# Optimization experiments

Measured on AMD Instinct MI355X. Metric: run time of the kernel, lower is better.

The kernel has to match this reference:

```python
import jax, jax.numpy as jnp
import numpy as np

B, S, H = 8, 1024, 1024
NH, DH = 16, 64
F_DIM, E, TOPK = 4096, 8, 2
EPS = 1e-5


def setup_inputs() -> dict:
    key = jax.random.key(0)
    ks = jax.random.split(key, 12)
    s = 0.02
    return {
        "x": jax.random.normal(ks[0], (B, S, H), jnp.float32),
        "ln1_w": jnp.ones((H,), jnp.float32),
        "ln1_b": jnp.zeros((H,), jnp.float32),
        "ln2_w": jnp.ones((H,), jnp.float32),
        "ln2_b": jnp.zeros((H,), jnp.float32),
        "in_proj_w": jax.random.normal(ks[1], (3 * H, H), jnp.float32) * s,
        "in_proj_b": jnp.zeros((3 * H,), jnp.float32),
        "out_proj_w": jax.random.normal(ks[2], (H, H), jnp.float32) * s,
        "out_proj_b": jnp.zeros((H,), jnp.float32),
        "gate_w": jax.random.normal(ks[3], (E, H), jnp.float32) * s,
        "gate_b": jnp.zeros((E,), jnp.float32),
        "w1": jax.random.normal(ks[4], (E, H, F_DIM), jnp.float32) * s,
        "b1": jnp.zeros((E, F_DIM), jnp.float32),
        "w2": jax.random.normal(ks[5], (E, F_DIM, H), jnp.float32) * s,
        "b2": jnp.zeros((E, H), jnp.float32),
    }


def _layernorm(x, w, b):
    mu = jnp.mean(x, axis=-1, keepdims=True)
    var = jnp.var(x, axis=-1, keepdims=True)
    return (x - mu) * jax.lax.rsqrt(var + EPS) * w + b


def reference(x, ln1_w, ln1_b, ln2_w, ln2_b, in_proj_w, in_proj_b,
              out_proj_w, out_proj_b, gate_w, gate_b, w1, b1, w2, b2):
    # --- attention sub-block ---
    xn = _layernorm(x, ln1_w, ln1_b)
    qkv = xn @ in_proj_w.T + in_proj_b                     # [B,S,3H]
    q, k, v = jnp.split(qkv, 3, axis=-1)
    q = q.reshape(B, S, NH, DH).transpose(0, 2, 1, 3)      # [B,NH,S,DH]
    k = k.reshape(B, S, NH, DH).transpose(0, 2, 1, 3)
    v = v.reshape(B, S, NH, DH).transpose(0, 2, 1, 3)
    scores = jnp.einsum("bhqd,bhkd->bhqk", q, k) / jnp.sqrt(jnp.float32(DH))
    attn = jax.nn.softmax(scores, axis=-1)
    ctx = jnp.einsum("bhqk,bhkd->bhqd", attn, v)
    ctx = ctx.transpose(0, 2, 1, 3).reshape(B, S, H)
    x = x + ctx @ out_proj_w.T + out_proj_b

    # --- MoE sub-block (dense compute-all-experts, top-k combine) ---
    xn2 = _layernorm(x, ln2_w, ln2_b)
    logits = xn2 @ gate_w.T + gate_b                       # [B,S,E]
    topk_vals, topk_idx = jax.lax.top_k(logits, TOPK)      # [B,S,K]
    probs = jax.nn.softmax(topk_vals, axis=-1)
    hid = jax.nn.gelu(jnp.einsum("bsh,ehf->bsef", xn2, w1) + b1, approximate=False)
    expert_out = jnp.einsum("bsef,efh->bseh", hid, w2) + b2  # [B,S,E,H]
    selected = jnp.take_along_axis(expert_out, topk_idx[..., None], axis=2)  # [B,S,K,H]
    moe_out = jnp.sum(probs[..., None] * selected, axis=2)
    return x + moe_out
```

## Files before the change

kernel.cpp:

```cpp
#include <hip/hip_runtime.h>
#include <math.h>

typedef unsigned short u16;
typedef short short8 __attribute__((ext_vector_type(8)));
typedef float f32x4 __attribute__((ext_vector_type(4)));
typedef unsigned short us4 __attribute__((ext_vector_type(4)));

#define NTOK 8192
#define NEXP 8

__device__ __forceinline__ u16 f2bf(float f) {
  union { float f; unsigned u; } v; v.f = f;
  unsigned r = v.u + 0x7FFFu + ((v.u >> 16) & 1u);
  return (u16)(r >> 16);
}
__device__ __forceinline__ float bf2f(u16 u) {
  union { unsigned u; float f; } v; v.u = ((unsigned)u) << 16; return v.f;
}
__device__ __forceinline__ void gload16(const u16* src, u16* ldsDst) {
  __builtin_amdgcn_global_load_lds(
    (const __attribute__((address_space(1))) unsigned int*)(const void*)src,
    (__attribute__((address_space(3))) unsigned int*)(void*)ldsDst, 16, 0, 0);
}
__device__ __forceinline__ float gelu_f(float v) {
  float ax = fabsf(v) * 0.70710678f;
  float t = __builtin_amdgcn_rcpf(1.0f + 0.3275911f * ax);
  float p = t * (0.254829592f + t * (-0.284496736f + t * (1.421413741f +
            t * (-1.453152027f + t * 1.061405429f))));
  float er = 1.0f - p * __expf(-ax * ax);
  er = copysignf(er, v);
  return 0.5f * v * (1.0f + er);
}

__global__ void cast_kernel(const float* __restrict__ in, u16* __restrict__ out, int n4) {
  int i = blockIdx.x * blockDim.x + threadIdx.x;
  if (i < n4) {
    float4 v = ((const float4*)in)[i];
    us4 o;
    o[0] = f2bf(v.x); o[1] = f2bf(v.y); o[2] = f2bf(v.z); o[3] = f2bf(v.w);
    ((us4*)out)[i] = o;
  }
}

__global__ void transpose_cast(const float* __restrict__ in, u16* __restrict__ out, int R, int C) {
  __shared__ float tile[64][65];
  const size_t eoff = (size_t)blockIdx.z * (size_t)R * (size_t)C;
  in += eoff; out += eoff;
  const int rb = blockIdx.y * 64, cb = blockIdx.x * 64;
  const int tid = threadIdx.x;
  const int lr4 = tid >> 4;
  const int lc4 = (tid & 15) * 4;
#pragma unroll
  for (int p = 0; p < 4; ++p) {
    float4 v = *(const float4*)&in[(size_t)(rb + p * 16 + lr4) * C + cb + lc4];
    tile[p * 16 + lr4][lc4 + 0] = v.x;
    tile[p * 16 + lr4][lc4 + 1] = v.y;
    tile[p * 16 + lr4][lc4 + 2] = v.z;
    tile[p * 16 + lr4][lc4 + 3] = v.w;
  }
  __syncthreads();
  const int oc = tid >> 3;
  const int orr = (tid & 7) * 8;
#pragma unroll
  for (int p = 0; p < 2; ++p) {
    int c = p * 32 + oc;
    short8 o;
#pragma unroll
    for (int j = 0; j < 8; ++j) o[j] = (short)f2bf(tile[orr + j][c]);
    *(short8*)&out[(size_t)(cb + c) * R + rb + orr] = o;
  }
}

__global__ void ln1_kernel(const float* __restrict__ x, const float* __restrict__ w,
                           const float* __restrict__ b, u16* __restrict__ xn) {
  const int t = blockIdx.x, tid = threadIdx.x;
  __shared__ float red[8];
  float4 v = ((const float4*)(x + (size_t)t * 1024))[tid];
  float s  = v.x + v.y + v.z + v.w;
  float sq = v.x*v.x + v.y*v.y + v.z*v.z + v.w*v.w;
#pragma unroll
  for (int m = 1; m < 64; m <<= 1) { s += __shfl_xor(s, m, 64); sq += __shfl_xor(sq, m, 64); }
  if ((tid & 63) == 0) { red[tid >> 6] = s; red[4 + (tid >> 6)] = sq; }
  __syncthreads();
  float S = red[0] + red[1] + red[2] + red[3];
  float Q = red[4] + red[5] + red[6] + red[7];
  float mu  = S * (1.0f / 1024.0f);
  float var = Q * (1.0f / 1024.0f) - mu * mu;
  float inv = rsqrtf(var + 1e-5f);
  float4 wv = ((const float4*)w)[tid];
  float4 bv = ((const float4*)b)[tid];
  us4 o;
  o[0] = f2bf((v.x - mu) * inv * wv.x + bv.x);
  o[1] = f2bf((v.y - mu) * inv * wv.y + bv.y);
  o[2] = f2bf((v.z - mu) * inv * wv.z + bv.z);
  o[3] = f2bf((v.w - mu) * inv * wv.w + bv.w);
  ((us4*)(xn + (size_t)t * 1024))[tid] = o;
}

__global__ void ln2_gate_kernel(const float* __restrict__ x2, const float* __restrict__ w,
                                const float* __restrict__ b, const float* __restrict__ gw,
                                const float* __restrict__ gb, u16* __restrict__ xn2,
                                int* __restrict__ cnt, int* __restrict__ list_tok,
                                float* __restrict__ list_prob, int* __restrict__ tok2slot) {
  const int t = blockIdx.x, tid = threadIdx.x;
  __shared__ float red[8];
  __shared__ float logits[NEXP];
  __shared__ float xrow[1024];
  float4 v = ((const float4*)(x2 + (size_t)t * 1024))[tid];
  float s  = v.x + v.y + v.z + v.w;
  float sq = v.x*v.x + v.y*v.y + v.z*v.z + v.w*v.w;
#pragma unroll
  for (int m = 1; m < 64; m <<= 1) { s += __shfl_xor(s, m, 64); sq += __shfl_xor(sq, m, 64); }
  if ((tid & 63) == 0) { red[tid >> 6] = s; red[4 + (tid >> 6)] = sq; }
  __syncthreads();
  float S = red[0] + red[1] + red[2] + red[3];
  float Q = red[4] + red[5] + red[6] + red[7];
  float mu  = S * (1.0f / 1024.0f);
  float var = Q * (1.0f / 1024.0f) - mu * mu;
  float inv = rsqrtf(var + 1e-5f);
  float4 wv = ((const float4*)w)[tid];
  float4 bv = ((const float4*)b)[tid];
  float n0 = (v.x - mu) * inv * wv.x + bv.x;
  float n1 = (v.y - mu) * inv * wv.y + bv.y;
  float n2 = (v.z - mu) * inv * wv.z + bv.z;
  float n3 = (v.w - mu) * inv * wv.w + bv.w;
  xrow[tid*4+0] = n0; xrow[tid*4+1] = n1; xrow[tid*4+2] = n2; xrow[tid*4+3] = n3;
  us4 o; o[0] = f2bf(n0); o[1] = f2bf(n1); o[2] = f2bf(n2); o[3] = f2bf(n3);
  ((us4*)(xn2 + (size_t)t * 1024))[tid] = o;
  __syncthreads();
  int e = tid >> 5, l32 = tid & 31;
  const float* gwe = gw + e * 1024;
  float part = 0.0f;
  for (int i = l32; i < 1024; i += 32) part += xrow[i] * gwe[i];
#pragma unroll
  for (int m = 1; m < 32; m <<= 1) part += __shfl_xor(part, m, 64);
  if (l32 == 0) logits[e] = part + gb[e];
  __syncthreads();
  if (tid == 0) {
    float v0 = -1e30f; int e0 = 0;
#pragma unroll
    for (int i = 0; i < NEXP; ++i) { float L = logits[i]; if (L > v0) { v0 = L; e0 = i; } }
    float v1 = -1e30f; int e1 = 0;
#pragma unroll
    for (int i = 0; i < NEXP; ++i) { if (i == e0) continue; float L = logits[i]; if (L > v1) { v1 = L; e1 = i; } }
    float texp = expf(v1 - v0);
    float p0 = 1.0f / (1.0f + texp);
    float p1 = texp / (1.0f + texp);
    int s0 = atomicAdd(&cnt[e0], 1);
    list_tok[e0 * NTOK + s0] = t; list_prob[e0 * NTOK + s0] = p0;
    int s1 = atomicAdd(&cnt[e1], 1);
    list_tok[e1 * NTOK + s1] = t; list_prob[e1 * NTOK + s1] = p1;
    if (tok2slot) {
      tok2slot[2 * t]     = e0 * NTOK + s0;
      tok2slot[2 * t + 1] = e1 * NTOK + s1;
    }
  }
}

__global__ void plan_kernel(const int* __restrict__ cnt, int* __restrict__ meta) {
  if (threadIdx.x == 0) {
    int base = 0, p = 0;
    for (int e = 0; e < NEXP; ++e) {
      meta[e] = base;
      int c = cnt[e];
      base += c;
      int nm = (c + 127) >> 7;
      for (int i = 0; i < nm; ++i) { meta[16 + 2 * p] = e; meta[17 + 2 * p] = i << 7; ++p; }
    }
    meta[8] = p;
  }
}

__launch_bounds__(256)
__global__ void attn_kernel(const u16* __restrict__ qkv, u16* __restrict__ ctx) {
  const int bh = blockIdx.y;
  const int b = bh >> 4, h = bh & 15;
  const int q0 = blockIdx.x * 64;
  const int tokBase = b * 1024;
  __shared__ __align__(16) u16 Qs[64 * 72];
  __shared__ __align__(16) u16 Ks[64 * 72];
  __shared__ __align__(16) u16 Vts[64 * 72];
  __shared__ __align__(16) u16 Ps[64 * 72];
  const int tid = threadIdx.x;
  const int wave = tid >> 6, lane = tid & 63, g = lane >> 4, lr = lane & 15;

  {
    int r = tid >> 2, d0 = (tid & 3) * 16;
    const u16* src = qkv + (size_t)(tokBase + q0 + r) * 3072 + h * 64 + d0;
    *(short8*)&Qs[r * 72 + d0]     = *(const short8*)src;
    *(short8*)&Qs[r * 72 + d0 + 8] = *(const short8*)(src + 8);
  }
  __syncthreads();
  short8 aq0 = *(const short8*)&Qs[(wave * 16 + lr) * 72 + g * 8];
  short8 aq1 = *(const short8*)&Qs[(wave * 16 + lr) * 72 + 32 + g * 8];

  const f32x4 zf = {0.f, 0.f, 0.f, 0.f};
  f32x4 Ofr[4] = {zf, zf, zf, zf};
  float m_run[4], l_run[4];
#pragma unroll
  for (int r = 0; r < 4; ++r) { m_run[r] = -1e30f; l_run[r] = 0.f; }

  for (int kt = 0; kt < 1024; kt += 64) {
    __syncthreads();
    {
      int r = tid >> 2, d0 = (tid & 3) * 16;
      const u16* ksrc = qkv + (size_t)(tokBase + kt + r) * 3072 + 1024 + h * 64 + d0;
      *(short8*)&Ks[r * 72 + d0]     = *(const short8*)ksrc;
      *(short8*)&Ks[r * 72 + d0 + 8] = *(const short8*)(ksrc + 8);
      const u16* vsrc = qkv + (size_t)(tokBase + kt + r) * 3072 + 2048 + h * 64 + d0;
      short8 v0 = *(const short8*)vsrc, v1 = *(const short8*)(vsrc + 8);
#pragma unroll
      for (int j = 0; j < 8; ++j) Vts[(d0 + j) * 72 + r] = (u16)v0[j];
#pragma unroll
      for (int j = 0; j < 8; ++j) Vts[(d0 + 8 + j) * 72 + r] = (u16)v1[j];
    }
    __syncthreads();
    f32x4 sf[4];
#pragma unroll
    for (int n = 0; n < 4; ++n) sf[n] = zf;
#pragma unroll
    for (int n = 0; n < 4; ++n) {
      short8 bk0 = *(const short8*)&Ks[(n * 16 + lr) * 72 + g * 8];
      short8 bk1 = *(const short8*)&Ks[(n * 16 + lr) * 72 + 32 + g * 8];
      sf[n] = __builtin_amdgcn_mfma_f32_16x16x32_bf16(aq0, bk0, sf[n], 0, 0, 0);
      sf[n] = __builtin_amdgcn_mfma_f32_16x16x32_bf16(aq1, bk1, sf[n], 0, 0, 0);
    }
#pragma unroll
    for (int n = 0; n < 4; ++n)
#pragma unroll
      for (int r = 0; r < 4; ++r) sf[n][r] *= 0.125f;
    float mnew[4], sc[4];
#pragma unroll
    for (int r = 0; r < 4; ++r) {
      float t0 = fmaxf(fmaxf(sf[0][r], sf[1][r]), fmaxf(sf[2][r], sf[3][r]));
#pragma unroll
      for (int msk = 1; msk < 16; msk <<= 1) t0 = fmaxf(t0, __shfl_xor(t0, msk, 64));
      mnew[r] = fmaxf(m_run[r], t0);
      sc[r] = __expf(m_run[r] - mnew[r]);
      m_run[r] = mnew[r];
    }
#pragma unroll
    for (int n = 0; n < 4; ++n)
#pragma unroll
      for (int r = 0; r < 4; ++r) sf[n][r] = __expf(sf[n][r] - mnew[r]);
#pragma unroll
    for (int r = 0; r < 4; ++r) {
      float s0 = sf[0][r] + sf[1][r] + sf[2][r] + sf[3][r];
#pragma unroll
      for (int msk = 1; msk < 16; msk <<= 1) s0 += __shfl_xor(s0, msk, 64);
      l_run[r] = l_run[r] * sc[r] + s0;
    }
#pragma unroll
    for (int nd = 0; nd < 4; ++nd)
#pragma unroll
      for (int r = 0; r < 4; ++r) Ofr[nd][r] *= sc[r];
#pragma unroll
    for (int n = 0; n < 4; ++n)
#pragma unroll
      for (int r = 0; r < 4; ++r)
        Ps[(wave * 16 + g * 4 + r) * 72 + n * 16 + lr] = f2bf(sf[n][r]);
    __syncthreads();
    short8 ap0 = *(const short8*)&Ps[(wave * 16 + lr) * 72 + g * 8];
    short8 ap1 = *(const short8*)&Ps[(wave * 16 + lr) * 72 + 32 + g * 8];
#pragma unroll
    for (int nd = 0; nd < 4; ++nd) {
      short8 bv0 = *(const short8*)&Vts[(nd * 16 + lr) * 72 + g * 8];
      short8 bv1 = *(const short8*)&Vts[(nd * 16 + lr) * 72 + 32 + g * 8];
      Ofr[nd] = __builtin_amdgcn_mfma_f32_16x16x32_bf16(ap0, bv0, Ofr[nd], 0, 0, 0);
      Ofr[nd] = __builtin_amdgcn_mfma_f32_16x16x32_bf16(ap1, bv1, Ofr[nd], 0, 0, 0);
    }
  }
#pragma unroll
  for (int nd = 0; nd < 4; ++nd)
#pragma unroll
    for (int r = 0; r < 4; ++r) {
      int tok = tokBase + q0 + wave * 16 + g * 4 + r;
      int col = h * 64 + nd * 16 + lr;
      ctx[(size_t)tok * 1024 + col] = f2bf(Ofr[nd][r] / l_run[r]);
    }
}

template<int EPI>
__launch_bounds__(256)
__global__ void gemm128(const u16* __restrict__ Abase, const u16* __restrict__ Bbase,
                        int K, int lda, int N, int ldc,
                        const float* __restrict__ bias,
                        const float* __restrict__ resid,
                        float* __restrict__ outF,
                        u16* __restrict__ outB,
                        const int* __restrict__ cnt,
                        const int* __restrict__ meta,
                        const int* __restrict__ list_tok,
                        const float* __restrict__ list_prob) {
  const int gx = gridDim.x, gy = gridDim.y;
  int nwg = gx * gy;
  int orig = blockIdx.x + blockIdx.y * gx;
  int q8 = nwg >> 3, r8 = nwg & 7, xcd = orig & 7, lid = orig >> 3;
  int wg = (xcd < r8 ? xcd * (q8 + 1) : r8 * (q8 + 1) + (xcd - r8) * q8) + lid;
  const int bx = wg % gx, by = wg / gx;
  const int n0 = bx * 128;

  int m0, e = 0, M = NTOK, slotBase = 0;
  const u16* Bw = Bbase;
  const float* biasp = bias;
  if constexpr (EPI >= 2) {
    if (by >= meta[8]) return;
    e = meta[16 + 2 * by];
    m0 = meta[17 + 2 * by];
    M = cnt[e];
    slotBase = meta[e];
    Bw += (size_t)e * (size_t)N * (size_t)K;
    biasp = bias + (size_t)e * N;
  } else {
    m0 = by * 128;
  }

  __shared__ __align__(16) u16 As[2][8192];
  __shared__ __align__(16) u16 Bs[2][8192];

  const int tid = threadIdx.x;
  const int wave = tid >> 6, lane = tid & 63, g = lane >> 4, lr = lane & 15;
  const int wm = wave >> 1, wn = wave & 1;

  unsigned aoff[4], boff[4];
#pragma unroll
  for (int i = 0; i < 4; ++i) {
    int ci = i * 256 + tid;
    int row = ci >> 3, c = ci & 7;
    int lc = c ^ (row & 7);
    int arow;
    if constexpr (EPI == 2) {
      int ridx = m0 + row; if (ridx > M - 1) ridx = M - 1;
      arow = list_tok[e * NTOK + ridx];
    } else if constexpr (EPI >= 3) {
      int ridx = m0 + row; if (ridx > M - 1) ridx = M - 1;
      arow = slotBase + ridx;
    } else {
      arow = m0 + row;
    }
    aoff[i] = (unsigned)arow * (unsigned)lda + (unsigned)(lc << 3);
    boff[i] = (unsigned)(n0 + row) * (unsigned)K + (unsigned)(lc << 3);
  }

  const int NT = K >> 6;

#define STAGE(T) do { int _t = (T); if (_t < NT) { int _b = _t & 1; int _kt = _t << 6; \
    _Pragma("unroll") for (int i = 0; i < 4; ++i) { \
      gload16(Abase + aoff[i] + _kt, &As[_b][(i * 256 + wave * 64) << 3]); \
      gload16(Bw + boff[i] + _kt, &Bs[_b][(i * 256 + wave * 64) << 3]); } } } while (0)

  const int sw = lr & 7;
  const int arb = (wm * 64 + lr) * 64;
  const int brb = (wn * 64 + lr) * 64;
  const int sk0 = (g ^ sw) * 8;
  const int sk1 = ((4 + g) ^ sw) * 8;

  const f32x4 zf = {0.f, 0.f, 0.f, 0.f};
  f32x4 acc[4][4];
#pragma unroll
  for (int m = 0; m < 4; ++m)
#pragma unroll
    for (int n = 0; n < 4; ++n) acc[m][n] = zf;

  STAGE(0);
  asm volatile("s_waitcnt vmcnt(0)" ::: "memory");
  __builtin_amdgcn_s_barrier();

  for (int t = 0; t < NT; ++t) {
    STAGE(t + 1);
    const u16* Ab = As[t & 1];
    const u16* Bb = Bs[t & 1];
    short8 af[4][2], bf[4][2];
#pragma unroll
    for (int m = 0; m < 4; ++m) {
      af[m][0] = *(const short8*)&Ab[arb + m * 1024 + sk0];
      af[m][1] = *(const short8*)&Ab[arb + m * 1024 + sk1];
    }
#pragma unroll
    for (int n = 0; n < 4; ++n) {
      bf[n][0] = *(const short8*)&Bb[brb + n * 1024 + sk0];
      bf[n][1] = *(const short8*)&Bb[brb + n * 1024 + sk1];
    }
    __builtin_amdgcn_s_setprio(1);
#pragma unroll
    for (int kk = 0; kk < 2; ++kk)
#pragma unroll
      for (int m = 0; m < 4; ++m)
#pragma unroll
        for (int n = 0; n < 4; ++n)
          acc[m][n] = __builtin_amdgcn_mfma_f32_16x16x32_bf16(af[m][kk], bf[n][kk], acc[m][n], 0, 0, 0);
    __builtin_amdgcn_s_setprio(0);
    asm volatile("s_waitcnt vmcnt(0)" ::: "memory");
    __builtin_amdgcn_s_barrier();
  }
#undef STAGE

#pragma unroll
  for (int m = 0; m < 4; ++m) {
    int rloc = wm * 64 + m * 16 + g * 4;
#pragma unroll
    for (int n = 0; n < 4; ++n) {
      int gc = n0 + wn * 64 + n * 16 + lr;
      float bcol = biasp[gc];
#pragma unroll
      for (int r = 0; r < 4; ++r) {
        int ridx = m0 + rloc + r;
        float vv = acc[m][n][r] + bcol;
        if constexpr (EPI == 0) {
          outB[(size_t)ridx * ldc + gc] = f2bf(vv);
        } else if constexpr (EPI == 1) {
          size_t off = (size_t)ridx * ldc + gc;
          outF[off] = vv + resid[off];
        } else if constexpr (EPI == 2) {
          if (ridx < M)
            outB[(size_t)(slotBase + ridx) * ldc + gc] = f2bf(gelu_f(vv));
        } else if constexpr (EPI == 3) {
          if (ridx < M)
            outB[(size_t)(slotBase + ridx) * ldc + gc] = f2bf(vv);
        } else {
          if (ridx < M) {
            int tok = list_tok[e * NTOK + ridx];
            float p = list_prob[e * NTOK + ridx];
            atomicAdd(&outF[(size_t)tok * ldc + gc], vv * p);
          }
        }
      }
    }
  }
}

__global__ void combine_kernel(const u16* __restrict__ part, const int* __restrict__ cnt,
                               const int* __restrict__ tok2slot, const float* __restrict__ lprb,
                               float* __restrict__ out) {
  const int t = blockIdx.x, tid = threadIdx.x;
  __shared__ int base[NEXP];
  if (tid == 0) {
    int b = 0;
#pragma unroll
    for (int j = 0; j < NEXP; ++j) { base[j] = b; b += cnt[j]; }
  }
  __syncthreads();
  int c0 = tok2slot[2 * t], c1 = tok2slot[2 * t + 1];
  float p0 = lprb[c0], p1 = lprb[c1];
  int g0 = base[c0 >> 13] + (c0 & 8191);
  int g1 = base[c1 >> 13] + (c1 & 8191);
  us4 a = ((const us4*)(part + (size_t)g0 * 1024))[tid];
  us4 b = ((const us4*)(part + (size_t)g1 * 1024))[tid];
  float4 o = ((const float4*)(out + (size_t)t * 1024))[tid];
  o.x += p0 * bf2f(a[0]) + p1 * bf2f(b[0]);
  o.y += p0 * bf2f(a[1]) + p1 * bf2f(b[1]);
  o.z += p0 * bf2f(a[2]) + p1 * bf2f(b[2]);
  o.w += p0 * bf2f(a[3]) + p1 * bf2f(b[3]);
  ((float4*)(out + (size_t)t * 1024))[tid] = o;
}

extern "C" void kernel_launch(void* const* d_in, const int* in_sizes, int n_in,
                              void* d_out, int out_size, void* d_ws, size_t ws_size,
                              hipStream_t stream) {
  const float* x    = (const float*)d_in[0];
  const float* ln1w = (const float*)d_in[1];
  const float* ln1b = (const float*)d_in[2];
  const float* ln2w = (const float*)d_in[3];
  const float* ln2b = (const float*)d_in[4];
  const float* inw  = (const float*)d_in[5];
  const float* inb  = (const float*)d_in[6];
  const float* outw = (const float*)d_in[7];
  const float* outb = (const float*)d_in[8];
  const float* gw   = (const float*)d_in[9];
  const float* gb   = (const float*)d_in[10];
  const float* w1   = (const float*)d_in[11];
  const float* b1   = (const float*)d_in[12];
  const float* w2   = (const float*)d_in[13];
  const float* b2   = (const float*)d_in[14];
  float* out = (float*)d_out;
  char* ws = (char*)d_ws;

  u16* xn1 = (u16*)(ws + 0);
  u16* qkv = (u16*)(ws + 16777216);
  u16* ctx = (u16*)(ws + 67108864);
  u16* hid = (u16*)(ws + 0);
  u16* xn2 = (u16*)(ws + 134217728);
  u16* w1t = (u16*)(ws + 150994944);
  u16* winb  = (u16*)(ws + 218103808);
  u16* woutb = (u16*)(ws + 224395264);
  u16* w2t = (u16*)(ws + 134217728);
  u16* part = (u16*)(ws + 201326592);

  const bool bigWS = ws_size >= 235475456ull;
  int *cnt, *meta, *ltok, *t2s; float* lprb;
  if (bigWS) {
    cnt  = (int*)(ws + 234881024);
    meta = (int*)(ws + 234883072);
    ltok = (int*)(ws + 234887168);
    lprb = (float*)(ws + 235149312);
    t2s  = (int*)(ws + 235411456);
  } else {
    cnt  = (int*)(ws + 226492416);
    meta = (int*)(ws + 226494464);
    ltok = (int*)(ws + 226498560);
    lprb = (float*)(ws + 226760704);
    t2s  = nullptr;
  }

  cast_kernel<<<3072, 256, 0, stream>>>(inw, winb, 786432);
  cast_kernel<<<1024, 256, 0, stream>>>(outw, woutb, 262144);
  transpose_cast<<<dim3(64, 16, 8), 256, 0, stream>>>(w1, w1t, 1024, 4096);

  ln1_kernel<<<8192, 256, 0, stream>>>(x, ln1w, ln1b, xn1);
  gemm128<0><<<dim3(24, 64), 256, 0, stream>>>(xn1, winb, 1024, 1024, 3072, 3072,
                                               inb, nullptr, nullptr, qkv, nullptr, nullptr, nullptr, nullptr);
  attn_kernel<<<dim3(16, 128), 256, 0, stream>>>(qkv, ctx);
  gemm128<1><<<dim3(8, 64), 256, 0, stream>>>(ctx, woutb, 1024, 1024, 1024, 1024,
                                              outb, x, out, nullptr, nullptr, nullptr, nullptr, nullptr);

  hipMemsetAsync(cnt, 0, 32, stream);
  ln2_gate_kernel<<<8192, 256, 0, stream>>>(out, ln2w, ln2b, gw, gb, xn2, cnt, ltok, lprb, t2s);
  plan_kernel<<<1, 64, 0, stream>>>(cnt, meta);
  gemm128<2><<<dim3(32, 136), 256, 0, stream>>>(xn2, w1t, 1024, 1024, 4096, 4096,
                                                b1, nullptr, nullptr, hid, cnt, meta, ltok, lprb);
  transpose_cast<<<dim3(16, 64, 8), 256, 0, stream>>>(w2, w2t, 4096, 1024);
  if (bigWS) {
    gemm128<3><<<dim3(8, 136), 256, 0, stream>>>(hid, w2t, 4096, 4096, 1024, 1024,
                                                 b2, nullptr, nullptr, part, cnt, meta, ltok, lprb);
    combine_kernel<<<8192, 256, 0, stream>>>(part, cnt, t2s, lprb, out);
  } else {
    gemm128<4><<<dim3(8, 136), 256, 0, stream>>>(hid, w2t, 4096, 4096, 1024, 1024,
                                                 b2, nullptr, out, nullptr, cnt, meta, ltok, lprb);
  }
}
```

Before: 1.115 ms.

## Rewrite GEMMs as 128x256 tiles with 8 waves and interleaved load/MFMA pipeline

Replaces the 128x128, 4-wave GEMM with a 128x256 tile kernel using 8 waves (512 threads) and a larger B buffer in LDS. The main loop is split into four quarter phases that interleave LDS fragment reads, MFMA bursts and global prefetches two tiles ahead, with partial vmcnt waits instead of a full drain every iteration. It also adds an M-major workgroup ordering for most GEMMs to improve weight reuse in L2. This is meant to reduce load latency stalls and raise MFMA utilisation, but it adds many barriers per iteration and limits occupancy to one block per CU.

```diff
diff --git a/kernel.cpp b/kernel.cpp
--- a/kernel.cpp
+++ b/kernel.cpp
@@ -280,25 +280,26 @@
     }
 }
 
-template<int EPI>
-__launch_bounds__(256)
-__global__ void gemm128(const u16* __restrict__ Abase, const u16* __restrict__ Bbase,
-                        int K, int lda, int N, int ldc,
-                        const float* __restrict__ bias,
-                        const float* __restrict__ resid,
-                        float* __restrict__ outF,
-                        u16* __restrict__ outB,
-                        const int* __restrict__ cnt,
-                        const int* __restrict__ meta,
-                        const int* __restrict__ list_tok,
-                        const float* __restrict__ list_prob) {
+template<int EPI, bool MMAJOR>
+__launch_bounds__(512, 1)
+__global__ void gemmT(const u16* __restrict__ Abase, const u16* __restrict__ Bbase,
+                      int K, int lda, int N, int ldc,
+                      const float* __restrict__ bias,
+                      const float* __restrict__ resid,
+                      float* __restrict__ outF,
+                      u16* __restrict__ outB,
+                      const int* __restrict__ cnt,
+                      const int* __restrict__ meta,
+                      const int* __restrict__ list_tok,
+                      const float* __restrict__ list_prob) {
   const int gx = gridDim.x, gy = gridDim.y;
   int nwg = gx * gy;
   int orig = blockIdx.x + blockIdx.y * gx;
   int q8 = nwg >> 3, r8 = nwg & 7, xcd = orig & 7, lid = orig >> 3;
   int wg = (xcd < r8 ? xcd * (q8 + 1) : r8 * (q8 + 1) + (xcd - r8) * q8) + lid;
-  const int bx = wg % gx, by = wg / gx;
-  const int n0 = bx * 128;
+  int bx, by;
+  if (MMAJOR) { by = wg % gy; bx = wg / gy; } else { bx = wg % gx; by = wg / gx; }
+  const int n0 = bx * 256;
 
   int m0, e = 0, M = NTOK, slotBase = 0;
   const u16* Bw = Bbase;
@@ -316,16 +317,16 @@
   }
 
   __shared__ __align__(16) u16 As[2][8192];
-  __shared__ __align__(16) u16 Bs[2][8192];
+  __shared__ __align__(16) u16 Bs[2][16384];
 
   const int tid = threadIdx.x;
   const int wave = tid >> 6, lane = tid & 63, g = lane >> 4, lr = lane & 15;
-  const int wm = wave >> 1, wn = wave & 1;
-
-  unsigned aoff[4], boff[4];
-#pragma unroll
-  for (int i = 0; i < 4; ++i) {
-    int ci = i * 256 + tid;
+  const int wm = wave >> 2, wn = wave & 3;
+
+  unsigned aoff[2], boff[4];
+#pragma unroll
+  for (int i = 0; i < 2; ++i) {
+    int ci = i * 512 + tid;
     int row = ci >> 3, c = ci & 7;
     int lc = c ^ (row & 7);
     int arow;
@@ -339,15 +340,23 @@
       arow = m0 + row;
     }
     aoff[i] = (unsigned)arow * (unsigned)lda + (unsigned)(lc << 3);
+  }
+#pragma unroll
+  for (int i = 0; i < 4; ++i) {
+    int ci = i * 512 + tid;
+    int row = ci >> 3, c = ci & 7;
+    int lc = c ^ (row & 7);
     boff[i] = (unsigned)(n0 + row) * (unsigned)K + (unsigned)(lc << 3);
   }
 
   const int NT = K >> 6;
 
-#define STAGE(T) do { int _t = (T); if (_t < NT) { int _b = _t & 1; int _kt = _t << 6; \
-    _Pragma("unroll") for (int i = 0; i < 4; ++i) { \
-      gload16(Abase + aoff[i] + _kt, &As[_b][(i * 256 + wave * 64) << 3]); \
-      gload16(Bw + boff[i] + _kt, &Bs[_b][(i * 256 + wave * 64) << 3]); } } } while (0)
+#define S_A(T) do { int _t = (T); if (_t < NT) { int _b = _t & 1; int _kt = _t << 6; \
+    gload16(Abase + aoff[0] + _kt, &As[_b][(0 * 512 + wave * 64) << 3]); \
+    gload16(Abase + aoff[1] + _kt, &As[_b][(1 * 512 + wave * 64) << 3]); } } while (0)
+#define S_B(T) do { int _t = (T); if (_t < NT) { int _b = _t & 1; int _kt = _t << 6; \
+    _Pragma("unroll") for (int i = 0; i < 4; ++i) \
+      gload16(Bw + boff[i] + _kt, &Bs[_b][(i * 512 + wave * 64) << 3]); } } while (0)
 
   const int sw = lr & 7;
   const int arb = (wm * 64 + lr) * 64;
@@ -362,38 +371,89 @@
 #pragma unroll
     for (int n = 0; n < 4; ++n) acc[m][n] = zf;
 
-  STAGE(0);
-  asm volatile("s_waitcnt vmcnt(0)" ::: "memory");
+  S_B(0); S_A(0); S_B(1); S_A(1);
+  if (NT >= 2) { asm volatile("s_waitcnt vmcnt(6)" ::: "memory"); }
+  else         { asm volatile("s_waitcnt vmcnt(0)" ::: "memory"); }
   __builtin_amdgcn_s_barrier();
 
   for (int t = 0; t < NT; ++t) {
-    STAGE(t + 1);
     const u16* Ab = As[t & 1];
     const u16* Bb = Bs[t & 1];
-    short8 af[4][2], bf[4][2];
-#pragma unroll
-    for (int m = 0; m < 4; ++m) {
-      af[m][0] = *(const short8*)&Ab[arb + m * 1024 + sk0];
-      af[m][1] = *(const short8*)&Ab[arb + m * 1024 + sk1];
-    }
-#pragma unroll
-    for (int n = 0; n < 4; ++n) {
-      bf[n][0] = *(const short8*)&Bb[brb + n * 1024 + sk0];
-      bf[n][1] = *(const short8*)&Bb[brb + n * 1024 + sk1];
-    }
+    short8 afr[2][2], bfr[4][2];
+#pragma unroll
+    for (int m = 0; m < 2; ++m) {
+      afr[m][0] = *(const short8*)&Ab[arb + m * 1024 + sk0];
+      afr[m][1] = *(const short8*)&Ab[arb + m * 1024 + sk1];
+    }
+#pragma unroll
+    for (int n = 0; n < 2; ++n) {
+      bfr[n][0] = *(const short8*)&Bb[brb + n * 1024 + sk0];
+      bfr[n][1] = *(const short8*)&Bb[brb + n * 1024 + sk1];
+    }
+    __builtin_amdgcn_s_barrier();
+    asm volatile("s_waitcnt lgkmcnt(0)" ::: "memory");
     __builtin_amdgcn_s_setprio(1);
 #pragma unroll
     for (int kk = 0; kk < 2; ++kk)
 #pragma unroll
-      for (int m = 0; m < 4; ++m)
-#pragma unroll
-        for (int n = 0; n < 4; ++n)
-          acc[m][n] = __builtin_amdgcn_mfma_f32_16x16x32_bf16(af[m][kk], bf[n][kk], acc[m][n], 0, 0, 0);
+      for (int m = 0; m < 2; ++m)
+#pragma unroll
+        for (int n = 0; n < 2; ++n)
+          acc[m][n] = __builtin_amdgcn_mfma_f32_16x16x32_bf16(afr[m][kk], bfr[n][kk], acc[m][n], 0, 0, 0);
     __builtin_amdgcn_s_setprio(0);
-    asm volatile("s_waitcnt vmcnt(0)" ::: "memory");
-    __builtin_amdgcn_s_barrier();
-  }
-#undef STAGE
+    __builtin_amdgcn_s_barrier();
+#pragma unroll
+    for (int n = 2; n < 4; ++n) {
+      bfr[n][0] = *(const short8*)&Bb[brb + n * 1024 + sk0];
+      bfr[n][1] = *(const short8*)&Bb[brb + n * 1024 + sk1];
+    }
+    __builtin_amdgcn_s_barrier();
+    asm volatile("s_waitcnt lgkmcnt(0)" ::: "memory");
+    __builtin_amdgcn_s_setprio(1);
+#pragma unroll
+    for (int kk = 0; kk < 2; ++kk)
+#pragma unroll
+      for (int m = 0; m < 2; ++m)
+#pragma unroll
+        for (int n = 2; n < 4; ++n)
+          acc[m][n] = __builtin_amdgcn_mfma_f32_16x16x32_bf16(afr[m][kk], bfr[n][kk], acc[m][n], 0, 0, 0);
+    __builtin_amdgcn_s_setprio(0);
+    __builtin_amdgcn_s_barrier();
+#pragma unroll
+    for (int m = 0; m < 2; ++m) {
+      afr[m][0] = *(const short8*)&Ab[arb + (m + 2) * 1024 + sk0];
+      afr[m][1] = *(const short8*)&Ab[arb + (m + 2) * 1024 + sk1];
+    }
+    S_B(t + 2);
+    __builtin_amdgcn_s_barrier();
+    asm volatile("s_waitcnt lgkmcnt(0)" ::: "memory");
+    __builtin_amdgcn_s_setprio(1);
+#pragma unroll
+    for (int kk = 0; kk < 2; ++kk)
+#pragma unroll
+      for (int m = 0; m < 2; ++m)
+#pragma unroll
+        for (int n = 0; n < 2; ++n)
+          acc[m + 2][n] = __builtin_amdgcn_mfma_f32_16x16x32_bf16(afr[m][kk], bfr[n][kk], acc[m + 2][n], 0, 0, 0);
+    __builtin_amdgcn_s_setprio(0);
+    __builtin_amdgcn_s_barrier();
+    S_A(t + 2);
+    if (t < NT - 2) { asm volatile("s_waitcnt vmcnt(6)" ::: "memory"); }
+    else            { asm volatile("s_waitcnt vmcnt(0)" ::: "memory"); }
+    __builtin_amdgcn_s_barrier();
+    __builtin_amdgcn_s_setprio(1);
+#pragma unroll
+    for (int kk = 0; kk < 2; ++kk)
+#pragma unroll
+      for (int m = 0; m < 2; ++m)
+#pragma unroll
+        for (int n = 2; n < 4; ++n)
+          acc[m + 2][n] = __builtin_amdgcn_mfma_f32_16x16x32_bf16(afr[m][kk], bfr[n][kk], acc[m + 2][n], 0, 0, 0);
+    __builtin_amdgcn_s_setprio(0);
+    __builtin_amdgcn_s_barrier();
+  }
+#undef S_A
+#undef S_B
 
 #pragma unroll
   for (int m = 0; m < 4; ++m) {
@@ -507,24 +567,24 @@
   transpose_cast<<<dim3(64, 16, 8), 256, 0, stream>>>(w1, w1t, 1024, 4096);
 
   ln1_kernel<<<8192, 256, 0, stream>>>(x, ln1w, ln1b, xn1);
-  gemm128<0><<<dim3(24, 64), 256, 0, stream>>>(xn1, winb, 1024, 1024, 3072, 3072,
-                                               inb, nullptr, nullptr, qkv, nullptr, nullptr, nullptr, nullptr);
+  gemmT<0, true><<<dim3(12, 64), 512, 0, stream>>>(xn1, winb, 1024, 1024, 3072, 3072,
+      inb, nullptr, nullptr, qkv, nullptr, nullptr, nullptr, nullptr);
   attn_kernel<<<dim3(16, 128), 256, 0, stream>>>(qkv, ctx);
-  gemm128<1><<<dim3(8, 64), 256, 0, stream>>>(ctx, woutb, 1024, 1024, 1024, 1024,
-                                              outb, x, out, nullptr, nullptr, nullptr, nullptr, nullptr);
+  gemmT<1, true><<<dim3(4, 64), 512, 0, stream>>>(ctx, woutb, 1024, 1024, 1024, 1024,
+      outb, x, out, nullptr, nullptr, nullptr, nullptr, nullptr);
 
   hipMemsetAsync(cnt, 0, 32, stream);
   ln2_gate_kernel<<<8192, 256, 0, stream>>>(out, ln2w, ln2b, gw, gb, xn2, cnt, ltok, lprb, t2s);
   plan_kernel<<<1, 64, 0, stream>>>(cnt, meta);
-  gemm128<2><<<dim3(32, 136), 256, 0, stream>>>(xn2, w1t, 1024, 1024, 4096, 4096,
-                                                b1, nullptr, nullptr, hid, cnt, meta, ltok, lprb);
+  gemmT<2, true><<<dim3(16, 136), 512, 0, stream>>>(xn2, w1t, 1024, 1024, 4096, 4096,
+      b1, nullptr, nullptr, hid, cnt, meta, ltok, lprb);
   transpose_cast<<<dim3(16, 64, 8), 256, 0, stream>>>(w2, w2t, 4096, 1024);
   if (bigWS) {
-    gemm128<3><<<dim3(8, 136), 256, 0, stream>>>(hid, w2t, 4096, 4096, 1024, 1024,
-                                                 b2, nullptr, nullptr, part, cnt, meta, ltok, lprb);
+    gemmT<3, false><<<dim3(4, 136), 512, 0, stream>>>(hid, w2t, 4096, 4096, 1024, 1024,
+        b2, nullptr, nullptr, part, cnt, meta, ltok, lprb);
     combine_kernel<<<8192, 256, 0, stream>>>(part, cnt, t2s, lprb, out);
   } else {
-    gemm128<4><<<dim3(8, 136), 256, 0, stream>>>(hid, w2t, 4096, 4096, 1024, 1024,
-                                                 b2, nullptr, out, nullptr, cnt, meta, ltok, lprb);
-  }
-}
+    gemmT<4, false><<<dim3(4, 136), 512, 0, stream>>>(hid, w2t, 4096, 4096, 1024, 1024,
+        b2, nullptr, out, nullptr, cnt, meta, ltok, lprb);
+  }
+}
```

New measurement: 1.187 ms. 6.5% more time.

## Make GEMM kernels persistent over M-slots with cross-tile prefetch pipeline

Applied to the files above, without the earlier changes.

The per-tile GEMM becomes a semi-persistent kernel. Each workgroup loops over a contiguous range of M-slots for a fixed N column, and the next slot's first K tiles are prefetched while the current tile's epilogue runs. The pipeline now keeps two stages in flight with vmcnt(8) instead of fully draining each iteration, and launch bounds ask for two workgroups per CU. The aim is to remove per-block launch and prologue cost and to overlap epilogue stores with loads, at the price of larger grids of fewer blocks, which can cause load imbalance and register pressure.

```diff
diff --git a/kernel.cpp b/kernel.cpp
--- a/kernel.cpp
+++ b/kernel.cpp
@@ -281,79 +281,91 @@
 }
 
 template<int EPI>
-__launch_bounds__(256)
-__global__ void gemm128(const u16* __restrict__ Abase, const u16* __restrict__ Bbase,
-                        int K, int lda, int N, int ldc,
-                        const float* __restrict__ bias,
-                        const float* __restrict__ resid,
-                        float* __restrict__ outF,
-                        u16* __restrict__ outB,
-                        const int* __restrict__ cnt,
-                        const int* __restrict__ meta,
-                        const int* __restrict__ list_tok,
-                        const float* __restrict__ list_prob) {
-  const int gx = gridDim.x, gy = gridDim.y;
-  int nwg = gx * gy;
-  int orig = blockIdx.x + blockIdx.y * gx;
+__launch_bounds__(256, 2)
+__global__ void gemmP(const u16* __restrict__ Abase, const u16* __restrict__ Bbase,
+                      int K, int lda, int N, int ldc, int nSlotsFixed,
+                      const float* __restrict__ bias,
+                      const float* __restrict__ resid,
+                      float* __restrict__ outF,
+                      u16* __restrict__ outB,
+                      const int* __restrict__ cnt,
+                      const int* __restrict__ meta,
+                      const int* __restrict__ list_tok,
+                      const float* __restrict__ list_prob) {
+  const int gx = gridDim.x, G = gridDim.y;
+  const int nwg = gx * G;
+  int orig = blockIdx.y + blockIdx.x * G;
   int q8 = nwg >> 3, r8 = nwg & 7, xcd = orig & 7, lid = orig >> 3;
   int wg = (xcd < r8 ? xcd * (q8 + 1) : r8 * (q8 + 1) + (xcd - r8) * q8) + lid;
-  const int bx = wg % gx, by = wg / gx;
+  const int bx = wg / G, gidx = wg % G;
   const int n0 = bx * 128;
 
-  int m0, e = 0, M = NTOK, slotBase = 0;
-  const u16* Bw = Bbase;
-  const float* biasp = bias;
-  if constexpr (EPI >= 2) {
-    if (by >= meta[8]) return;
-    e = meta[16 + 2 * by];
-    m0 = meta[17 + 2 * by];
-    M = cnt[e];
-    slotBase = meta[e];
-    Bw += (size_t)e * (size_t)N * (size_t)K;
-    biasp = bias + (size_t)e * N;
-  } else {
-    m0 = by * 128;
-  }
+  const int S = (EPI >= 2) ? meta[8] : nSlotsFixed;
+  const int cpb = (S + G - 1) / G;
+  const int sBeg = gidx * cpb;
+  int sEnd = sBeg + cpb; if (sEnd > S) sEnd = S;
+  if (sBeg >= sEnd) return;
+  const int nslots = sEnd - sBeg;
+  const int NT = K >> 6;
+  const int ntLog = 31 - __builtin_clz((unsigned)NT);
+  const int nIt = nslots << ntLog;
 
   __shared__ __align__(16) u16 As[2][8192];
   __shared__ __align__(16) u16 Bs[2][8192];
 
   const int tid = threadIdx.x;
-  const int wave = tid >> 6, lane = tid & 63, g = lane >> 4, lr = lane & 15;
+  const int wave = tid >> 6, lane = tid & 63, gp = lane >> 4, lr = lane & 15;
   const int wm = wave >> 1, wn = wave & 1;
 
-  unsigned aoff[4], boff[4];
+  unsigned boff[4];
 #pragma unroll
   for (int i = 0; i < 4; ++i) {
     int ci = i * 256 + tid;
     int row = ci >> 3, c = ci & 7;
     int lc = c ^ (row & 7);
-    int arow;
-    if constexpr (EPI == 2) {
-      int ridx = m0 + row; if (ridx > M - 1) ridx = M - 1;
-      arow = list_tok[e * NTOK + ridx];
-    } else if constexpr (EPI >= 3) {
-      int ridx = m0 + row; if (ridx > M - 1) ridx = M - 1;
-      arow = slotBase + ridx;
+    boff[i] = (unsigned)(n0 + row) * (unsigned)K + (unsigned)(lc << 3);
+  }
+
+  int eC, m0C, MC, sbC; const u16* BwC; unsigned aoffC[4];
+  int eN, m0N, MN, sbN; const u16* BwN; unsigned aoffN[4];
+
+  auto loadSlot = [&](int s, int& e, int& m0, int& M, int& sb, const u16*& Bw, unsigned (&ao)[4]) {
+    if constexpr (EPI >= 2) {
+      e = meta[16 + 2 * s]; m0 = meta[17 + 2 * s]; M = cnt[e]; sb = meta[e];
+      Bw = Bbase + (size_t)e * (size_t)N * (size_t)K;
     } else {
-      arow = m0 + row;
-    }
-    aoff[i] = (unsigned)arow * (unsigned)lda + (unsigned)(lc << 3);
-    boff[i] = (unsigned)(n0 + row) * (unsigned)K + (unsigned)(lc << 3);
-  }
-
-  const int NT = K >> 6;
-
-#define STAGE(T) do { int _t = (T); if (_t < NT) { int _b = _t & 1; int _kt = _t << 6; \
-    _Pragma("unroll") for (int i = 0; i < 4; ++i) { \
-      gload16(Abase + aoff[i] + _kt, &As[_b][(i * 256 + wave * 64) << 3]); \
-      gload16(Bw + boff[i] + _kt, &Bs[_b][(i * 256 + wave * 64) << 3]); } } } while (0)
+      e = 0; m0 = s * 128; M = NTOK; sb = 0; Bw = Bbase;
+    }
+#pragma unroll
+    for (int i = 0; i < 4; ++i) {
+      int ci = i * 256 + tid;
+      int row = ci >> 3, c = ci & 7;
+      int lc = c ^ (row & 7);
+      int arow;
+      if constexpr (EPI == 2) {
+        int r = m0 + row; if (r > M - 1) r = M - 1;
+        arow = list_tok[e * NTOK + r];
+      } else if constexpr (EPI >= 3) {
+        int r = m0 + row; if (r > M - 1) r = M - 1;
+        arow = sb + r;
+      } else {
+        arow = m0 + row;
+      }
+      ao[i] = (unsigned)arow * (unsigned)lda + (unsigned)(lc << 3);
+    }
+  };
+
+  loadSlot(sBeg, eC, m0C, MC, sbC, BwC, aoffC);
+  if (nslots > 1) loadSlot(sBeg + 1, eN, m0N, MN, sbN, BwN, aoffN);
+  else { eN = eC; m0N = m0C; MN = MC; sbN = sbC; BwN = BwC;
+#pragma unroll
+         for (int i = 0; i < 4; ++i) aoffN[i] = aoffC[i]; }
 
   const int sw = lr & 7;
   const int arb = (wm * 64 + lr) * 64;
   const int brb = (wn * 64 + lr) * 64;
-  const int sk0 = (g ^ sw) * 8;
-  const int sk1 = ((4 + g) ^ sw) * 8;
+  const int sk0 = (gp ^ sw) * 8;
+  const int sk1 = ((4 + gp) ^ sw) * 8;
 
   const f32x4 zf = {0.f, 0.f, 0.f, 0.f};
   f32x4 acc[4][4];
@@ -362,14 +374,23 @@
 #pragma unroll
     for (int n = 0; n < 4; ++n) acc[m][n] = zf;
 
-  STAGE(0);
-  asm volatile("s_waitcnt vmcnt(0)" ::: "memory");
+#pragma unroll
+  for (int tt = 0; tt < 2; ++tt) {
+    int kt = tt << 6;
+#pragma unroll
+    for (int i = 0; i < 4; ++i) {
+      gload16(Abase + aoffC[i] + kt, &As[tt][(i * 256 + wave * 64) << 3]);
+      gload16(BwC + boff[i] + kt, &Bs[tt][(i * 256 + wave * 64) << 3]);
+    }
+  }
+  asm volatile("s_waitcnt vmcnt(8)" ::: "memory");
   __builtin_amdgcn_s_barrier();
 
-  for (int t = 0; t < NT; ++t) {
-    STAGE(t + 1);
-    const u16* Ab = As[t & 1];
-    const u16* Bb = Bs[t & 1];
+  for (int it = 0; it < nIt; ++it) {
+    const int sRel = it >> ntLog;
+    const int t = it & (NT - 1);
+    const u16* Ab = As[it & 1];
+    const u16* Bb = Bs[it & 1];
     short8 af[4][2], bf[4][2];
 #pragma unroll
     for (int m = 0; m < 4; ++m) {
@@ -381,6 +402,23 @@
       bf[n][0] = *(const short8*)&Bb[brb + n * 1024 + sk0];
       bf[n][1] = *(const short8*)&Bb[brb + n * 1024 + sk1];
     }
+    asm volatile("s_waitcnt lgkmcnt(0)" ::: "memory");
+    __builtin_amdgcn_s_barrier();
+    {
+      int it2 = it + 2;
+      if (it2 < nIt) {
+        bool nx = (it2 >> ntLog) != sRel;
+        int kt2 = (it2 & (NT - 1)) << 6;
+        int b2 = it2 & 1;
+#pragma unroll
+        for (int i = 0; i < 4; ++i) {
+          unsigned ao = nx ? aoffN[i] : aoffC[i];
+          const u16* bw = nx ? BwN : BwC;
+          gload16(Abase + ao + kt2, &As[b2][(i * 256 + wave * 64) << 3]);
+          gload16(bw + boff[i] + kt2, &Bs[b2][(i * 256 + wave * 64) << 3]);
+        }
+      }
+    }
     __builtin_amdgcn_s_setprio(1);
 #pragma unroll
     for (int kk = 0; kk < 2; ++kk)
@@ -390,41 +428,51 @@
         for (int n = 0; n < 4; ++n)
           acc[m][n] = __builtin_amdgcn_mfma_f32_16x16x32_bf16(af[m][kk], bf[n][kk], acc[m][n], 0, 0, 0);
     __builtin_amdgcn_s_setprio(0);
-    asm volatile("s_waitcnt vmcnt(0)" ::: "memory");
+    if (it < nIt - 3) { asm volatile("s_waitcnt vmcnt(8)" ::: "memory"); }
+    else              { asm volatile("s_waitcnt vmcnt(0)" ::: "memory"); }
     __builtin_amdgcn_s_barrier();
-  }
-#undef STAGE
-
-#pragma unroll
-  for (int m = 0; m < 4; ++m) {
-    int rloc = wm * 64 + m * 16 + g * 4;
-#pragma unroll
-    for (int n = 0; n < 4; ++n) {
-      int gc = n0 + wn * 64 + n * 16 + lr;
-      float bcol = biasp[gc];
-#pragma unroll
-      for (int r = 0; r < 4; ++r) {
-        int ridx = m0 + rloc + r;
-        float vv = acc[m][n][r] + bcol;
-        if constexpr (EPI == 0) {
-          outB[(size_t)ridx * ldc + gc] = f2bf(vv);
-        } else if constexpr (EPI == 1) {
-          size_t off = (size_t)ridx * ldc + gc;
-          outF[off] = vv + resid[off];
-        } else if constexpr (EPI == 2) {
-          if (ridx < M)
-            outB[(size_t)(slotBase + ridx) * ldc + gc] = f2bf(gelu_f(vv));
-        } else if constexpr (EPI == 3) {
-          if (ridx < M)
-            outB[(size_t)(slotBase + ridx) * ldc + gc] = f2bf(vv);
-        } else {
-          if (ridx < M) {
-            int tok = list_tok[e * NTOK + ridx];
-            float p = list_prob[e * NTOK + ridx];
-            atomicAdd(&outF[(size_t)tok * ldc + gc], vv * p);
+
+    if (t == NT - 1) {
+#pragma unroll
+      for (int m = 0; m < 4; ++m) {
+        int rloc = wm * 64 + m * 16 + gp * 4;
+#pragma unroll
+        for (int n = 0; n < 4; ++n) {
+          int gc = n0 + wn * 64 + n * 16 + lr;
+          float bcol;
+          if constexpr (EPI >= 2) bcol = bias[(size_t)eC * N + gc];
+          else bcol = bias[gc];
+#pragma unroll
+          for (int r = 0; r < 4; ++r) {
+            int ridx = m0C + rloc + r;
+            float vv = acc[m][n][r] + bcol;
+            if constexpr (EPI == 0) {
+              outB[(size_t)ridx * ldc + gc] = f2bf(vv);
+            } else if constexpr (EPI == 1) {
+              size_t off = (size_t)ridx * ldc + gc;
+              outF[off] = vv + resid[off];
+            } else if constexpr (EPI == 2) {
+              if (ridx < MC)
+                outB[(size_t)(sbC + ridx) * ldc + gc] = f2bf(gelu_f(vv));
+            } else if constexpr (EPI == 3) {
+              if (ridx < MC)
+                outB[(size_t)(sbC + ridx) * ldc + gc] = f2bf(vv);
+            } else {
+              if (ridx < MC) {
+                int tok = list_tok[eC * NTOK + ridx];
+                float p = list_prob[eC * NTOK + ridx];
+                atomicAdd(&outF[(size_t)tok * ldc + gc], vv * p);
+              }
+            }
+            acc[m][n][r] = 0.f;
           }
         }
       }
+      eC = eN; m0C = m0N; MC = MN; sbC = sbN; BwC = BwN;
+#pragma unroll
+      for (int i = 0; i < 4; ++i) aoffC[i] = aoffN[i];
+      int s2 = sBeg + sRel + 2;
+      if (s2 < sEnd) loadSlot(s2, eN, m0N, MN, sbN, BwN, aoffN);
     }
   }
 }
@@ -507,24 +555,24 @@
   transpose_cast<<<dim3(64, 16, 8), 256, 0, stream>>>(w1, w1t, 1024, 4096);
 
   ln1_kernel<<<8192, 256, 0, stream>>>(x, ln1w, ln1b, xn1);
-  gemm128<0><<<dim3(24, 64), 256, 0, stream>>>(xn1, winb, 1024, 1024, 3072, 3072,
-                                               inb, nullptr, nullptr, qkv, nullptr, nullptr, nullptr, nullptr);
+  gemmP<0><<<dim3(24, 16), 256, 0, stream>>>(xn1, winb, 1024, 1024, 3072, 3072, 64,
+      inb, nullptr, nullptr, qkv, nullptr, nullptr, nullptr, nullptr);
   attn_kernel<<<dim3(16, 128), 256, 0, stream>>>(qkv, ctx);
-  gemm128<1><<<dim3(8, 64), 256, 0, stream>>>(ctx, woutb, 1024, 1024, 1024, 1024,
-                                              outb, x, out, nullptr, nullptr, nullptr, nullptr, nullptr);
+  gemmP<1><<<dim3(8, 32), 256, 0, stream>>>(ctx, woutb, 1024, 1024, 1024, 1024, 64,
+      outb, x, out, nullptr, nullptr, nullptr, nullptr, nullptr);
 
   hipMemsetAsync(cnt, 0, 32, stream);
   ln2_gate_kernel<<<8192, 256, 0, stream>>>(out, ln2w, ln2b, gw, gb, xn2, cnt, ltok, lprb, t2s);
   plan_kernel<<<1, 64, 0, stream>>>(cnt, meta);
-  gemm128<2><<<dim3(32, 136), 256, 0, stream>>>(xn2, w1t, 1024, 1024, 4096, 4096,
-                                                b1, nullptr, nullptr, hid, cnt, meta, ltok, lprb);
+  gemmP<2><<<dim3(32, 16), 256, 0, stream>>>(xn2, w1t, 1024, 1024, 4096, 4096, 0,
+      b1, nullptr, nullptr, hid, cnt, meta, ltok, lprb);
   transpose_cast<<<dim3(16, 64, 8), 256, 0, stream>>>(w2, w2t, 4096, 1024);
   if (bigWS) {
-    gemm128<3><<<dim3(8, 136), 256, 0, stream>>>(hid, w2t, 4096, 4096, 1024, 1024,
-                                                 b2, nullptr, nullptr, part, cnt, meta, ltok, lprb);
+    gemmP<3><<<dim3(8, 64), 256, 0, stream>>>(hid, w2t, 4096, 4096, 1024, 1024, 0,
+        b2, nullptr, nullptr, part, cnt, meta, ltok, lprb);
     combine_kernel<<<8192, 256, 0, stream>>>(part, cnt, t2s, lprb, out);
   } else {
-    gemm128<4><<<dim3(8, 136), 256, 0, stream>>>(hid, w2t, 4096, 4096, 1024, 1024,
-                                                 b2, nullptr, out, nullptr, cnt, meta, ltok, lprb);
-  }
-}
+    gemmP<4><<<dim3(8, 64), 256, 0, stream>>>(hid, w2t, 4096, 4096, 1024, 1024, 0,
+        b2, nullptr, out, nullptr, cnt, meta, ltok, lprb);
+  }
+}
```

Result: faster. 1.082 ms (-2.9%).
